# Performance work log

Measured on AMD Instinct MI355X. Metric: run time of the kernel, lower is better.

Reference implementation:

```python
import jax, jax.numpy as jnp
import numpy as np

B, D, T, STRIDE = 16, 512, 2048, 4
SIGMA_SQUARE = 5.0
L = -(-T // STRIDE)  # ceil(T/stride) = 512


def setup_inputs() -> dict:
    key = jax.random.key(0)
    k1, k2, k3 = jax.random.split(key, 3)
    x = jax.random.normal(k1, (B, D, T), dtype=jnp.float32)
    # score conv: Conv1d(hdim, 1, 1, bias=False) == a single weight vector over D
    # (zero-initialized in the module; use small random values for a meaningful test)
    w = jax.random.normal(k2, (D,), dtype=jnp.float32) * 0.01
    x_lengths = jax.random.randint(k3, (B,), T // 2, T + 1)
    x_mask = jnp.arange(T)[None, :] < x_lengths[:, None]  # [B, T] bool
    return {"x": x, "w": w, "x_mask": x_mask, "x_lengths": x_lengths}


def reference(x, w, x_mask, x_lengths):
    maskf = x_mask.astype(x.dtype)  # [B, T]
    z_lengths = jnp.ceil(x_lengths.astype(x.dtype) / STRIDE).astype(jnp.int32)  # [B]
    z_mask = x_mask[:, ::STRIDE]  # [B, L]

    # score = exp(conv1x1(x)) * mask ; cum-sum position score
    score = jnp.exp(jnp.einsum('bdt,d->bt', x, w)) * maskf  # [B, T]
    cum = jnp.cumsum(score, axis=-1)  # [B, T]
    norm = (cum - cum[:, :1]) / (cum[:, -1:] - cum[:, :1]) \
           * (z_lengths[:, None].astype(x.dtype) - 1.0)  # [B, T]

    # monotonic-rate regularizer (get_score_loss)
    diff = norm[:, 1:] - norm[:, :-1]  # [B, T-1]
    score_loss = ((jax.nn.relu(diff - 1.0) * maskf[:, 1:]).sum(axis=-1)
                  / (x_lengths.astype(x.dtype) - 1.0)).mean()

    # masked Gaussian distance -> softmax over T -> alignment-weighted sum
    idx = jnp.arange(L, dtype=x.dtype)  # [L]
    dist = -SIGMA_SQUARE * (idx[None, None, :] - norm[:, :, None]) ** 2  # [B, T, L]
    dist = jnp.swapaxes(dist, 1, 2)  # [B, L, T]
    dist = jnp.where(x_mask[:, None, :], dist, -jnp.inf)
    alignment = jax.nn.softmax(dist, axis=-1) * z_mask[:, :, None].astype(x.dtype)  # [B, L, T]

    z = jnp.einsum('blt,bdt->bdl', alignment, x)  # [B, D, L]
    return z, z_mask, z_lengths, alignment, score_loss
```

## Files before the change

kernel.cpp:

```cpp
#include <hip/hip_runtime.h>
#include <cstddef>

#define Bn 16
#define Dn 512
#define Tn 2048
#define Ln 512
#define NLT 64

__global__ __launch_bounds__(256) void scorefill_kernel(const float* __restrict__ x,
                                                        const float* __restrict__ w,
                                                        const int* __restrict__ xlen,
                                                        float* __restrict__ score,
                                                        float* __restrict__ align) {
    int bid = blockIdx.x;
    int tid = threadIdx.x;

    if (bid >= 1024) {
        int r0 = (bid - 1024) * 2;
        float4 z4 = make_float4(0.f, 0.f, 0.f, 0.f);
#pragma unroll
        for (int rr = 0; rr < 2; ++rr) {
            int r = r0 + rr;
            int b = r >> 9, l = r & 511;
            int zl = (xlen[b] + 3) >> 2;
            if (l < zl) continue;
            float4* row4 = (float4*)(align + (size_t)r * Tn);
            row4[tid]       = z4;
            row4[tid + 256] = z4;
        }
        return;
    }

    int b   = bid >> 6;
    int tc  = bid & 63;
    int xl  = xlen[b];
    int t0c = tc * 32;
    if (t0c >= xl) {
        if (tid < 8)
            *(float4*)&score[b * Tn + t0c + tid * 4] = make_float4(0.f, 0.f, 0.f, 0.f);
        return;
    }
    int tq = tid & 7;
    int dg = tid >> 3;
    int t0 = t0c + tq * 4;
    const float* xb = x + (size_t)b * Dn * Tn + (size_t)(dg * 16) * Tn + t0;
    const float* wb = w + dg * 16;

    float4 rx[16];
#pragma unroll
    for (int i = 0; i < 16; ++i)
        rx[i] = *(const float4*)&xb[(size_t)i * Tn];

    float4 acc = make_float4(0.f, 0.f, 0.f, 0.f);
#pragma unroll
    for (int i = 0; i < 16; ++i) {
        float wd = wb[i];
        acc.x = fmaf(rx[i].x, wd, acc.x);
        acc.y = fmaf(rx[i].y, wd, acc.y);
        acc.z = fmaf(rx[i].z, wd, acc.z);
        acc.w = fmaf(rx[i].w, wd, acc.w);
    }

    __shared__ float4 red[32][8];
    __shared__ float4 red2[8][8];
    red[dg][tq] = acc;
    __syncthreads();
    if (tid < 64) {
        int q = tid & 7, g = tid >> 3;
        float4 s0 = red[g * 4 + 0][q], s1 = red[g * 4 + 1][q];
        float4 s2 = red[g * 4 + 2][q], s3 = red[g * 4 + 3][q];
        float4 s;
        s.x = (s0.x + s1.x) + (s2.x + s3.x);
        s.y = (s0.y + s1.y) + (s2.y + s3.y);
        s.z = (s0.z + s1.z) + (s2.z + s3.z);
        s.w = (s0.w + s1.w) + (s2.w + s3.w);
        red2[g][q] = s;
    }
    __syncthreads();
    if (tid < 8) {
        float4 s = red2[0][tid];
#pragma unroll
        for (int g = 1; g < 8; ++g) {
            float4 r = red2[g][tid];
            s.x += r.x; s.y += r.y; s.z += r.z; s.w += r.w;
        }
        int t = t0c + tid * 4;
        float4 o;
        o.x = (t + 0 < xl) ? __expf(s.x) : 0.f;
        o.y = (t + 1 < xl) ? __expf(s.y) : 0.f;
        o.z = (t + 2 < xl) ? __expf(s.z) : 0.f;
        o.w = (t + 3 < xl) ? __expf(s.w) : 0.f;
        *(float4*)&score[b * Tn + t] = o;
    }
}

__global__ __launch_bounds__(256) void scan_kernel(const float* __restrict__ score,
                                                   const int* __restrict__ xlen,
                                                   float* __restrict__ norm,
                                                   float* __restrict__ loss_part,
                                                   float* __restrict__ zmask_out,
                                                   float* __restrict__ zlen_out,
                                                   int* __restrict__ wlo,
                                                   int* __restrict__ whi,
                                                   float* __restrict__ sMout,
                                                   float* __restrict__ sIout) {
    int b = blockIdx.x, tid = threadIdx.x;
    int xl = xlen[b];
    int zl = (xl + 3) >> 2;
    const float* sc = score + b * Tn;

    __shared__ float sNorm[Tn];
    __shared__ int   sTC[Ln];

    float v[8]; float s = 0.f;
#pragma unroll
    for (int k = 0; k < 8; ++k) { v[k] = sc[tid * 8 + k]; s += v[k]; }

    float ps = s;
#pragma unroll
    for (int off = 1; off < 64; off <<= 1) {
        float n = __shfl_up(ps, off, 64);
        if ((tid & 63) >= off) ps += n;
    }
    __shared__ float wsum[4];
    if ((tid & 63) == 63) wsum[tid >> 6] = ps;
    __syncthreads();
    float base = 0.f;
#pragma unroll
    for (int wv = 0; wv < 4; ++wv) if (wv < (tid >> 6)) base += wsum[wv];
    float total = wsum[0] + wsum[1] + wsum[2] + wsum[3];
    float cum0  = sc[0];
    float scale = (float)(zl - 1) / (total - cum0);

    float run = base + ps - s;
    float nv[8];
#pragma unroll
    for (int k = 0; k < 8; ++k) {
        run += v[k];
        float xx = (run - cum0) * scale;
        nv[k] = xx;
        norm[b * Tn + tid * 8 + k] = xx;
        sNorm[tid * 8 + k] = xx;
    }

    float ls = 0.f;
#pragma unroll
    for (int k = 0; k < 8; ++k) {
        int t = tid * 8 + k;
        if (t >= 1 && t < xl) {
            float diff = v[k] * scale;
            ls += fmaxf(diff - 1.0f, 0.f);
        }
    }
#pragma unroll
    for (int off = 32; off; off >>= 1) ls += __shfl_down(ls, off, 64);
    __shared__ float lw[4];
    if ((tid & 63) == 0) lw[tid >> 6] = ls;

    for (int l = tid; l < Ln; l += 256)
        zmask_out[b * Ln + l] = (l * 4 < xl) ? 1.f : 0.f;
    if (tid == 0) zlen_out[b] = (float)zl;

    for (int i = tid; i < NLT; i += 256) {
        wlo[b * NLT + i] = xl;
        whi[b * NLT + i] = xl;
    }
    for (int l = tid; l < Ln; l += 256) sTC[l] = xl - 1;
    __syncthreads();
    if (tid == 0) loss_part[b] = (lw[0] + lw[1] + lw[2] + lw[3]) / (float)(xl - 1);

#pragma unroll
    for (int k = 0; k < 8; ++k) {
        int t = tid * 8 + k;
        float vv = nv[k];
        float p  = (t == 0) ? -1e9f : sNorm[t - 1];
        int lsr = (int)floorf((p + 1.5f) * 0.125f) + 1; if (lsr < 0) lsr = 0;
        int ler = (int)floorf((vv + 1.5f) * 0.125f);    if (ler > NLT - 1) ler = NLT - 1;
        for (int lt = lsr; lt <= ler; ++lt) wlo[b * NLT + lt] = t;
        int hs = (int)ceilf((p - 8.5f) * 0.125f);       if (hs < 0) hs = 0;
        int he = (int)ceilf((vv - 8.5f) * 0.125f) - 1;  if (he > NLT - 1) he = NLT - 1;
        for (int lt = hs; lt <= he; ++lt) whi[b * NLT + lt] = t;
        int cs = (int)floorf(p) + 1;  if (cs < 0) cs = 0;
        int ce = (int)floorf(vv);     if (ce > Ln - 1) ce = Ln - 1;
        for (int l = cs; l <= ce; ++l) sTC[l] = t;
    }
    __syncthreads();

    for (int l = tid; l < Ln; l += 256) {
        float mv = 0.f, iv = 0.f;
        if (l < zl) {
            int tc2 = sTC[l];
            float d1 = (float)l - sNorm[tc2];
            float m  = -5.f * d1 * d1;
            if (tc2 > 0) { float d0v = (float)l - sNorm[tc2 - 1]; float c = -5.f * d0v * d0v; m = fmaxf(m, c); }
            int lo = (l >= 2) ? sTC[l - 2] : 0;
            int hi = (l + 2 <= zl - 1) ? sTC[l + 2] : xl;
            int tcm1 = (tc2 > 0) ? tc2 - 1 : 0;
            if (lo > tcm1) lo = tcm1;
            int tcp1 = (tc2 + 1 < xl) ? tc2 + 1 : xl;
            if (hi < tcp1) hi = tcp1;
            float ssum = 0.f;
            for (int t = lo; t < hi; ++t) {
                float df = (float)l - sNorm[t];
                ssum += __expf(-5.f * df * df - m);
            }
            mv = m; iv = 1.f / ssum;
        }
        sMout[b * Ln + l] = mv;
        sIout[b * Ln + l] = iv;
    }
}

__global__ __launch_bounds__(256) void z_kernel(const float* __restrict__ x,
                                                const float* __restrict__ norm,
                                                const int* __restrict__ xlen,
                                                const int* __restrict__ wlo,
                                                const int* __restrict__ whi,
                                                const float* __restrict__ sM,
                                                const float* __restrict__ sI,
                                                const float* __restrict__ loss_part,
                                                float* __restrict__ align,
                                                float* __restrict__ z,
                                                float* __restrict__ out_loss) {
    int tid = threadIdx.x;
    int bid = blockIdx.x;
    if (bid == 0 && tid == 0) {
        float s = 0.f;
        for (int i = 0; i < Bn; ++i) s += loss_part[i];
        out_loss[0] = s / (float)Bn;
    }
    int swz = (bid & 7) * 256 + (bid >> 3);
    int b   = swz >> 7;
    int rem = swz & 127;
    int lt  = rem >> 1;
    int dh  = rem & 1;
    int l0  = lt * 8;
    int xl  = xlen[b];
    int zl  = (xl + 3) >> 2;
    int d   = dh * 256 + tid;
    size_t zr = (size_t)(b * Dn + d) * Ln + l0;

    if (l0 >= zl) {
        float4 z4 = make_float4(0.f, 0.f, 0.f, 0.f);
        *(float4*)&z[zr] = z4; *(float4*)&z[zr + 4] = z4;
        return;
    }

    int tlo = wlo[b * NLT + lt];
    int thi = whi[b * NLT + lt];
    if (thi > xl) thi = xl;
    int tA = tlo & ~15;

    {
        int start4 = (thi + 3) & ~3;
        if (start4 > Tn) start4 = Tn;
        int rest   = Tn - start4 - tA;
        if (rest < 0) rest = 0;
        int mid4   = start4 + ((rest >> 3) << 2);
        int row    = tid >> 5, lane32 = tid & 31;
        float* arw = align + (size_t)(b * Ln + l0 + row) * Tn;
        float4 z4f = make_float4(0.f, 0.f, 0.f, 0.f);
        if (dh == 0) {
            for (int q = lane32; q < (tA >> 2); q += 32)
                ((float4*)arw)[q] = z4f;
            if (thi + lane32 < start4) arw[thi + lane32] = 0.f;
            for (int q = (start4 >> 2) + lane32; q < (mid4 >> 2); q += 32)
                ((float4*)arw)[q] = z4f;
        } else {
            for (int q = (mid4 >> 2) + lane32; q < (Tn >> 2); q += 32)
                ((float4*)arw)[q] = z4f;
        }
    }

    __shared__ float sA[64][8];
    const float* nb = norm + b * Tn;
    const float* xr = x + (size_t)(b * Dn + d) * Tn;

    int al = tid >> 5;
    int as = tid & 31;
    float ml = sM[b * Ln + l0 + al];
    float il = sI[b * Ln + l0 + al];
    float lr = (float)(l0 + al);
    float* ar = align + (size_t)(b * Ln + l0 + al) * Tn;

    float acc[8] = {};
    float4 rx[16];

    for (int t0 = tA; t0 < thi; t0 += 64) {
#pragma unroll
        for (int j = 0; j < 16; ++j) {
            int tj = t0 + 4 * j;
            if (tj > Tn - 4) tj = Tn - 4;
            rx[j] = *(const float4*)&xr[tj];
        }
        {
            int t1 = t0 + as, t2 = t1 + 32;
            float a1 = 0.f, a2 = 0.f;
            if (t1 < thi) { float df = lr - nb[t1]; a1 = __expf(fmaf(-5.f * df, df, -ml)) * il; }
            if (t2 < thi) { float df = lr - nb[t2]; a2 = __expf(fmaf(-5.f * df, df, -ml)) * il; }
            sA[as][al] = a1;
            sA[as + 32][al] = a2;
            if (dh == 0) {
                if (t1 < thi) ar[t1] = a1;
                if (t2 < thi) ar[t2] = a2;
            }
        }
        __syncthreads();
#pragma unroll
        for (int c = 0; c < 16; ++c) {
            float4 xv = rx[c];
#pragma unroll
            for (int e = 0; e < 4; ++e) {
                int s = 4 * c + e;
                float xs = ((const float*)&xv)[e];
                float4 a0 = *(const float4*)&sA[s][0];
                float4 a1 = *(const float4*)&sA[s][4];
                acc[0] = fmaf(xs, a0.x, acc[0]);
                acc[1] = fmaf(xs, a0.y, acc[1]);
                acc[2] = fmaf(xs, a0.z, acc[2]);
                acc[3] = fmaf(xs, a0.w, acc[3]);
                acc[4] = fmaf(xs, a1.x, acc[4]);
                acc[5] = fmaf(xs, a1.y, acc[5]);
                acc[6] = fmaf(xs, a1.z, acc[6]);
                acc[7] = fmaf(xs, a1.w, acc[7]);
            }
        }
        __syncthreads();
    }

    *(float4*)&z[zr]     = make_float4(acc[0], acc[1], acc[2], acc[3]);
    *(float4*)&z[zr + 4] = make_float4(acc[4], acc[5], acc[6], acc[7]);
}

extern "C" void kernel_launch(void* const* d_in, const int* in_sizes, int n_in,
                              void* d_out, int out_size, void* d_ws, size_t ws_size,
                              hipStream_t stream) {
    const float* x    = (const float*)d_in[0];
    const float* w    = (const float*)d_in[1];
    const int*   xlen = (const int*)d_in[3];
    float* out = (float*)d_out;

    const size_t OFF_Z     = 0;
    const size_t OFF_ZMASK = (size_t)Bn * Dn * Ln;
    const size_t OFF_ZLEN  = OFF_ZMASK + (size_t)Bn * Ln;
    const size_t OFF_ALIGN = OFF_ZLEN + Bn;
    const size_t OFF_LOSS  = OFF_ALIGN + (size_t)Bn * Ln * Tn;

    float* score     = (float*)d_ws;
    float* norm      = score + (size_t)Bn * Tn;
    float* loss_part = norm + (size_t)Bn * Tn;
    int*   wlo       = (int*)(loss_part + Bn);
    int*   whi       = wlo + Bn * NLT;
    float* sMw       = (float*)(whi + Bn * NLT);
    float* sIw       = sMw + (size_t)Bn * Ln;

    scorefill_kernel<<<1024 + 4096, 256, 0, stream>>>(x, w, xlen, score,
                                                      out + OFF_ALIGN);
    scan_kernel<<<Bn, 256, 0, stream>>>(score, xlen, norm, loss_part,
                                        out + OFF_ZMASK, out + OFF_ZLEN,
                                        wlo, whi, sMw, sIw);
    z_kernel<<<Bn * NLT * 2, 256, 0, stream>>>(x, norm, xlen, wlo, whi,
                                               sMw, sIw, loss_part,
                                               out + OFF_ALIGN, out + OFF_Z,
                                               out + OFF_LOSS);
}
```

Measured before the change: 52.81 us.

## Move align zero-fill into z kernel and widen scan to 1024 threads

Takes the zero-fill of the masked alignment rows out of the score kernel and appends it as extra blocks of the z kernel, so the score kernel only does the reduction and the fill runs alongside the main z work. The single-block-per-batch scan kernel now uses 1024 threads with two elements each instead of 256 threads with eight, which shortens the serial per-thread work in this latency-bound 16-block stage. The cost is a larger z launch and a 16-wave cross-warp reduction in the scan.

```diff
diff --git a/kernel.cpp b/kernel.cpp
--- a/kernel.cpp
+++ b/kernel.cpp
@@ -7,30 +7,12 @@
 #define Ln 512
 #define NLT 64
 
-__global__ __launch_bounds__(256) void scorefill_kernel(const float* __restrict__ x,
-                                                        const float* __restrict__ w,
-                                                        const int* __restrict__ xlen,
-                                                        float* __restrict__ score,
-                                                        float* __restrict__ align) {
+__global__ __launch_bounds__(256) void score_kernel(const float* __restrict__ x,
+                                                    const float* __restrict__ w,
+                                                    const int* __restrict__ xlen,
+                                                    float* __restrict__ score) {
     int bid = blockIdx.x;
     int tid = threadIdx.x;
-
-    if (bid >= 1024) {
-        int r0 = (bid - 1024) * 2;
-        float4 z4 = make_float4(0.f, 0.f, 0.f, 0.f);
-#pragma unroll
-        for (int rr = 0; rr < 2; ++rr) {
-            int r = r0 + rr;
-            int b = r >> 9, l = r & 511;
-            int zl = (xlen[b] + 3) >> 2;
-            if (l < zl) continue;
-            float4* row4 = (float4*)(align + (size_t)r * Tn);
-            row4[tid]       = z4;
-            row4[tid + 256] = z4;
-        }
-        return;
-    }
-
     int b   = bid >> 6;
     int tc  = bid & 63;
     int xl  = xlen[b];
@@ -94,16 +76,16 @@
     }
 }
 
-__global__ __launch_bounds__(256) void scan_kernel(const float* __restrict__ score,
-                                                   const int* __restrict__ xlen,
-                                                   float* __restrict__ norm,
-                                                   float* __restrict__ loss_part,
-                                                   float* __restrict__ zmask_out,
-                                                   float* __restrict__ zlen_out,
-                                                   int* __restrict__ wlo,
-                                                   int* __restrict__ whi,
-                                                   float* __restrict__ sMout,
-                                                   float* __restrict__ sIout) {
+__global__ __launch_bounds__(1024) void scan_kernel(const float* __restrict__ score,
+                                                    const int* __restrict__ xlen,
+                                                    float* __restrict__ norm,
+                                                    float* __restrict__ loss_part,
+                                                    float* __restrict__ zmask_out,
+                                                    float* __restrict__ zlen_out,
+                                                    int* __restrict__ wlo,
+                                                    int* __restrict__ whi,
+                                                    float* __restrict__ sMout,
+                                                    float* __restrict__ sIout) {
     int b = blockIdx.x, tid = threadIdx.x;
     int xl = xlen[b];
     int zl = (xl + 3) >> 2;
@@ -111,10 +93,10 @@
 
     __shared__ float sNorm[Tn];
     __shared__ int   sTC[Ln];
-
-    float v[8]; float s = 0.f;
-#pragma unroll
-    for (int k = 0; k < 8; ++k) { v[k] = sc[tid * 8 + k]; s += v[k]; }
+    __shared__ float wsum[16], lw[16];
+
+    float v0 = sc[2 * tid], v1 = sc[2 * tid + 1];
+    float s  = v0 + v1;
 
     float ps = s;
 #pragma unroll
@@ -122,57 +104,56 @@
         float n = __shfl_up(ps, off, 64);
         if ((tid & 63) >= off) ps += n;
     }
-    __shared__ float wsum[4];
     if ((tid & 63) == 63) wsum[tid >> 6] = ps;
     __syncthreads();
-    float base = 0.f;
-#pragma unroll
-    for (int wv = 0; wv < 4; ++wv) if (wv < (tid >> 6)) base += wsum[wv];
-    float total = wsum[0] + wsum[1] + wsum[2] + wsum[3];
+    float base = 0.f, total = 0.f;
+#pragma unroll
+    for (int w2 = 0; w2 < 16; ++w2) {
+        float t = wsum[w2];
+        if (w2 < (tid >> 6)) base += t;
+        total += t;
+    }
     float cum0  = sc[0];
     float scale = (float)(zl - 1) / (total - cum0);
 
     float run = base + ps - s;
-    float nv[8];
-#pragma unroll
-    for (int k = 0; k < 8; ++k) {
-        run += v[k];
-        float xx = (run - cum0) * scale;
-        nv[k] = xx;
-        norm[b * Tn + tid * 8 + k] = xx;
-        sNorm[tid * 8 + k] = xx;
-    }
+    float n0v = (run + v0 - cum0) * scale;
+    float n1v = (run + s  - cum0) * scale;
+    norm[b * Tn + 2 * tid]     = n0v;
+    norm[b * Tn + 2 * tid + 1] = n1v;
+    sNorm[2 * tid]     = n0v;
+    sNorm[2 * tid + 1] = n1v;
 
     float ls = 0.f;
-#pragma unroll
-    for (int k = 0; k < 8; ++k) {
-        int t = tid * 8 + k;
-        if (t >= 1 && t < xl) {
-            float diff = v[k] * scale;
-            ls += fmaxf(diff - 1.0f, 0.f);
-        }
+    {
+        int t = 2 * tid;
+        if (t >= 1 && t < xl) ls += fmaxf(v0 * scale - 1.0f, 0.f);
+        if (t + 1 < xl)       ls += fmaxf(v1 * scale - 1.0f, 0.f);
     }
 #pragma unroll
     for (int off = 32; off; off >>= 1) ls += __shfl_down(ls, off, 64);
-    __shared__ float lw[4];
     if ((tid & 63) == 0) lw[tid >> 6] = ls;
 
-    for (int l = tid; l < Ln; l += 256)
-        zmask_out[b * Ln + l] = (l * 4 < xl) ? 1.f : 0.f;
+    if (tid < Ln) {
+        zmask_out[b * Ln + tid] = (tid * 4 < xl) ? 1.f : 0.f;
+        sTC[tid] = xl - 1;
+    }
+    if (tid < NLT) {
+        wlo[b * NLT + tid] = xl;
+        whi[b * NLT + tid] = xl;
+    }
     if (tid == 0) zlen_out[b] = (float)zl;
-
-    for (int i = tid; i < NLT; i += 256) {
-        wlo[b * NLT + i] = xl;
-        whi[b * NLT + i] = xl;
-    }
-    for (int l = tid; l < Ln; l += 256) sTC[l] = xl - 1;
-    __syncthreads();
-    if (tid == 0) loss_part[b] = (lw[0] + lw[1] + lw[2] + lw[3]) / (float)(xl - 1);
-
-#pragma unroll
-    for (int k = 0; k < 8; ++k) {
-        int t = tid * 8 + k;
-        float vv = nv[k];
+    __syncthreads();
+    if (tid == 0) {
+        float t = 0.f;
+        for (int i = 0; i < 16; ++i) t += lw[i];
+        loss_part[b] = t / (float)(xl - 1);
+    }
+
+#pragma unroll
+    for (int k = 0; k < 2; ++k) {
+        int t = 2 * tid + k;
+        float vv = k ? n1v : n0v;
         float p  = (t == 0) ? -1e9f : sNorm[t - 1];
         int lsr = (int)floorf((p + 1.5f) * 0.125f) + 1; if (lsr < 0) lsr = 0;
         int ler = (int)floorf((vv + 1.5f) * 0.125f);    if (ler > NLT - 1) ler = NLT - 1;
@@ -186,7 +167,8 @@
     }
     __syncthreads();
 
-    for (int l = tid; l < Ln; l += 256) {
+    if (tid < Ln) {
+        int l = tid;
         float mv = 0.f, iv = 0.f;
         if (l < zl) {
             int tc2 = sTC[l];
@@ -224,6 +206,23 @@
                                                 float* __restrict__ out_loss) {
     int tid = threadIdx.x;
     int bid = blockIdx.x;
+
+    if (bid >= 2048) {
+        int r0 = (bid - 2048) * 2;
+        float4 z4 = make_float4(0.f, 0.f, 0.f, 0.f);
+#pragma unroll
+        for (int rr = 0; rr < 2; ++rr) {
+            int r = r0 + rr;
+            int b = r >> 9, l = r & 511;
+            int zl = (xlen[b] + 3) >> 2;
+            if (l < zl) continue;
+            float4* row4 = (float4*)(align + (size_t)r * Tn);
+            row4[tid]       = z4;
+            row4[tid + 256] = z4;
+        }
+        return;
+    }
+
     if (bid == 0 && tid == 0) {
         float s = 0.f;
         for (int i = 0; i < Bn; ++i) s += loss_part[i];
@@ -354,13 +353,12 @@
     float* sMw       = (float*)(whi + Bn * NLT);
     float* sIw       = sMw + (size_t)Bn * Ln;
 
-    scorefill_kernel<<<1024 + 4096, 256, 0, stream>>>(x, w, xlen, score,
-                                                      out + OFF_ALIGN);
-    scan_kernel<<<Bn, 256, 0, stream>>>(score, xlen, norm, loss_part,
-                                        out + OFF_ZMASK, out + OFF_ZLEN,
-                                        wlo, whi, sMw, sIw);
-    z_kernel<<<Bn * NLT * 2, 256, 0, stream>>>(x, norm, xlen, wlo, whi,
-                                               sMw, sIw, loss_part,
-                                               out + OFF_ALIGN, out + OFF_Z,
-                                               out + OFF_LOSS);
+    score_kernel<<<1024, 256, 0, stream>>>(x, w, xlen, score);
+    scan_kernel<<<Bn, 1024, 0, stream>>>(score, xlen, norm, loss_part,
+                                         out + OFF_ZMASK, out + OFF_ZLEN,
+                                         wlo, whi, sMw, sIw);
+    z_kernel<<<2048 + 4096, 256, 0, stream>>>(x, norm, xlen, wlo, whi,
+                                              sMw, sIw, loss_part,
+                                              out + OFF_ALIGN, out + OFF_Z,
+                                              out + OFF_LOSS);
 }
```

Measured after the change: 49.94 us. 5.4% less time.
